# Kernel tuning notes

Measured on AMD Instinct MI355X. Metric: run time of the kernel, lower is better.

Reference implementation:

```python
import jax, jax.numpy as jnp
import numpy as np

N_NODES = 100000
N_EDGES = 3200000
NFEAT = 512
NHID = 256
KEEP_PROB = 0.5  # dropout p = 0.5


def setup_inputs() -> dict:
    key = jax.random.key(0)
    ks = jax.random.split(key, 9)
    x = jax.random.normal(ks[0], (N_NODES, NFEAT), dtype=jnp.float32)
    W1 = jax.random.normal(ks[1], (NFEAT, NHID), dtype=jnp.float32) * (1.0 / np.sqrt(NFEAT))
    b1 = jax.random.normal(ks[2], (NHID,), dtype=jnp.float32) * 0.01
    W2 = jax.random.normal(ks[3], (NHID, NHID), dtype=jnp.float32) * (1.0 / np.sqrt(NHID))
    b2 = jax.random.normal(ks[4], (NHID,), dtype=jnp.float32) * 0.01
    edge_row = jnp.sort(jax.random.randint(ks[5], (N_EDGES,), 0, N_NODES, dtype=jnp.int64))
    edge_col = jax.random.randint(ks[6], (N_EDGES,), 0, N_NODES, dtype=jnp.int64)
    edge_weight = jax.random.uniform(ks[7], (N_EDGES,), dtype=jnp.float32)
    drop_u = jax.random.uniform(ks[8], (N_NODES, NHID), dtype=jnp.float32)
    return {"x": x, "W1": W1, "b1": b1, "W2": W2, "b2": b2,
            "edge_row": edge_row, "edge_col": edge_col,
            "edge_weight": edge_weight, "drop_u": drop_u}


def reference(x, W1, b1, W2, b2, edge_row, edge_col, edge_weight, drop_u):
    n = x.shape[0]

    def spmm(h):
        # out[i] = sum_j adj[i, j] * h[j]  (COO gather + segment-sum)
        msg = h[edge_col] * edge_weight[:, None]  # [E, d]
        return jax.ops.segment_sum(msg, edge_row, num_segments=n)

    # layer 1: relu(spmm(adj, x @ W1) + b1)
    h = jax.nn.relu(spmm(x @ W1) + b1)
    # deterministic dropout (training=True, p=0.5): keep where u < keep_prob, scale by 1/keep
    mask = (drop_u < KEEP_PROB).astype(h.dtype)
    h = h * mask / KEEP_PROB
    # layer 2: relu(spmm(adj, h @ W2) + b2)
    h = jax.nn.relu(spmm(h @ W2) + b2)
    return jax.nn.log_softmax(h, axis=1)
```

## Files before the change

kernel.cpp:

```cpp
#include <hip/hip_runtime.h>
#include <stdint.h>

#define N_NODES 100000
#define N_EDGES 3200000
#define NFEAT 512
#define NHID 256
#define MPAD 100096

typedef __attribute__((ext_vector_type(8))) short bf16x8_t;
typedef __attribute__((ext_vector_type(4))) float f32x4_t;

#define RFL(x) __builtin_amdgcn_readfirstlane(x)

__device__ inline unsigned short f2bf(float f) {
  union { float f; uint32_t u; } x; x.f = f;
  uint32_t r = x.u + 0x7fffu + ((x.u >> 16) & 1u);
  return (unsigned short)(r >> 16);
}
__device__ inline float b2f(unsigned short u) {
  union { uint32_t u; float f; } x; x.u = ((uint32_t)u) << 16;
  return x.f;
}

__global__ void prep_k(const float* __restrict__ W1, const float* __restrict__ W2,
                       unsigned short* __restrict__ W1T, unsigned short* __restrict__ W2T) {
  int i = blockIdx.x * 256 + threadIdx.x;
  if (i < NFEAT * NHID) {
    int k = i >> 8, n = i & 255;
    W1T[n * NFEAT + k] = f2bf(W1[i]);
  } else {
    int j = i - NFEAT * NHID;
    int k = j >> 8, n = j & 255;
    W2T[n * NHID + k] = f2bf(W2[j]);
  }
}

__global__ void rowptr_k(const int* __restrict__ erow, int* __restrict__ rowptr) {
  int r = blockIdx.x * 256 + threadIdx.x;
  if (r > N_NODES) return;
  int lo = 0, hi = N_EDGES;
  while (lo < hi) {
    int mid = (lo + hi) >> 1;
    if (erow[mid] < r) lo = mid + 1; else hi = mid;
  }
  rowptr[r] = lo;
}

template <bool A_FP32>
__global__ __launch_bounds__(512) void gemm_bt2(const void* __restrict__ Ap,
                                                const unsigned short* __restrict__ BT,
                                                unsigned short* __restrict__ C,
                                                int K, int Mreal) {
  __shared__ __align__(16) unsigned short As[128 * 64];
  __shared__ __align__(16) unsigned short Bs[256 * 64];
  const int tid = threadIdx.x;
  const int lane = tid & 63, wid = tid >> 6;
  const int wm = wid >> 2, wn = wid & 3;
  const int m0 = blockIdx.x * 128;
  const int lrow = lane & 15, lhi = lane >> 4;

  f32x4_t acc[4][4] = {};

  const int nt = K >> 6;
  for (int t = 0; t < nt; ++t) {
    __syncthreads();
    if constexpr (A_FP32) {
      const float* A = (const float*)Ap;
      const int rr = tid >> 4;
      const int kq = (tid & 15) << 2;
#pragma unroll
      for (int round = 0; round < 4; ++round) {
        int row = rr + (round << 5);
        int grow = m0 + row; grow = grow < Mreal ? grow : Mreal - 1;
        const float4 v = *(const float4*)(A + (size_t)grow * K + (t << 6) + kq);
        ushort4 b4;
        b4.x = f2bf(v.x); b4.y = f2bf(v.y); b4.z = f2bf(v.z); b4.w = f2bf(v.w);
        *(ushort4*)&As[(row << 6) + (kq ^ ((row & 7) << 3))] = b4;
      }
    } else {
      const unsigned short* A = (const unsigned short*)Ap;
      const int Lrow = tid >> 3;
      const int Lc = (tid & 7) << 4;
#pragma unroll
      for (int round = 0; round < 2; ++round) {
        int row = Lrow + (round << 6);
        int srcc = Lc ^ ((row & 7) << 4);
        const char* g = (const char*)(A + (size_t)(m0 + row) * K + (t << 6)) + srcc;
        __builtin_amdgcn_global_load_lds(
            (const __attribute__((address_space(1))) void*)g,
            (__attribute__((address_space(3))) void*)((char*)As + tid * 16 + (round << 13)),
            16, 0, 0);
      }
    }
    {
      const int Lrow = tid >> 3;
      const int Lc = (tid & 7) << 4;
#pragma unroll
      for (int round = 0; round < 4; ++round) {
        int row = Lrow + (round << 6);
        int srcc = Lc ^ ((row & 7) << 4);
        const char* g = (const char*)(BT + (size_t)row * K + (t << 6)) + srcc;
        __builtin_amdgcn_global_load_lds(
            (const __attribute__((address_space(1))) void*)g,
            (__attribute__((address_space(3))) void*)((char*)Bs + tid * 16 + (round << 13)),
            16, 0, 0);
      }
    }
    asm volatile("s_waitcnt vmcnt(0)" ::: "memory");
    __syncthreads();

#pragma unroll
    for (int ks = 0; ks < 2; ++ks) {
      bf16x8_t af[4], bfr[4];
      const int cu = (ks << 5) + (lhi << 3);
#pragma unroll
      for (int mf = 0; mf < 4; ++mf) {
        int row = (wm << 6) + (mf << 4) + lrow;
        af[mf] = *(const bf16x8_t*)&As[(row << 6) + (cu ^ ((row & 7) << 3))];
      }
#pragma unroll
      for (int nf = 0; nf < 4; ++nf) {
        int row = (wn << 6) + (nf << 4) + lrow;
        bfr[nf] = *(const bf16x8_t*)&Bs[(row << 6) + (cu ^ ((row & 7) << 3))];
      }
#pragma unroll
      for (int mf = 0; mf < 4; ++mf)
#pragma unroll
        for (int nf = 0; nf < 4; ++nf)
          acc[mf][nf] = __builtin_amdgcn_mfma_f32_16x16x32_bf16(af[mf], bfr[nf], acc[mf][nf], 0, 0, 0);
    }
  }

#pragma unroll
  for (int mf = 0; mf < 4; ++mf)
#pragma unroll
    for (int nf = 0; nf < 4; ++nf)
#pragma unroll
      for (int j = 0; j < 4; ++j) {
        int gm = m0 + (wm << 6) + (mf << 4) + (lhi << 2) + j;
        int gn = (wn << 6) + (nf << 4) + lrow;
        C[(size_t)gm * 256 + gn] = f2bf(acc[mf][nf][j]);
      }
}

__global__ __launch_bounds__(256) void spmm1_k(const unsigned short* __restrict__ XW1,
                                               const int* __restrict__ rowptr,
                                               const int* __restrict__ ecol,
                                               const float* __restrict__ ew,
                                               const float* __restrict__ b1,
                                               const float* __restrict__ du,
                                               unsigned short* __restrict__ H) {
  const int lane = threadIdx.x & 63, wid = threadIdx.x >> 6;
  const int r = blockIdx.x * 4 + wid;
  const uint32_t c8 = (uint32_t)lane << 3;
  const int c4 = lane << 2;
  if (r >= N_NODES) {
    ushort4 z; z.x = z.y = z.z = z.w = 0;
    *(ushort4*)&H[(size_t)r * 256 + c4] = z;
    return;
  }
  const char* Xb = (const char*)XW1;
  const float4 bb = *(const float4*)&b1[c4];
  const float4 u = *(const float4*)&du[(size_t)r * 256 + c4];
  float a0 = 0, a1 = 0, a2 = 0, a3 = 0;
  int e  = RFL(rowptr[r]);
  int e1 = RFL(rowptr[r + 1]);
  for (; e + 8 <= e1; e += 8) {
    ushort4 v[8]; float w[8];
#pragma unroll
    for (int q = 0; q < 8; ++q) {
      uint32_t c = (uint32_t)RFL(ecol[e + q]);
      w[q] = __uint_as_float(RFL(__float_as_uint(ew[e + q])));
      v[q] = *(const ushort4*)(Xb + ((c << 9) + c8));
    }
#pragma unroll
    for (int q = 0; q < 8; ++q) {
      a0 += w[q] * b2f(v[q].x); a1 += w[q] * b2f(v[q].y);
      a2 += w[q] * b2f(v[q].z); a3 += w[q] * b2f(v[q].w);
    }
  }
  for (; e < e1; ++e) {
    uint32_t c = (uint32_t)RFL(ecol[e]);
    float w = __uint_as_float(RFL(__float_as_uint(ew[e])));
    ushort4 v = *(const ushort4*)(Xb + ((c << 9) + c8));
    a0 += w * b2f(v.x); a1 += w * b2f(v.y); a2 += w * b2f(v.z); a3 += w * b2f(v.w);
  }
  float h0 = fmaxf(a0 + bb.x, 0.f) * (u.x < 0.5f ? 2.f : 0.f);
  float h1 = fmaxf(a1 + bb.y, 0.f) * (u.y < 0.5f ? 2.f : 0.f);
  float h2 = fmaxf(a2 + bb.z, 0.f) * (u.z < 0.5f ? 2.f : 0.f);
  float h3 = fmaxf(a3 + bb.w, 0.f) * (u.w < 0.5f ? 2.f : 0.f);
  ushort4 o; o.x = f2bf(h0); o.y = f2bf(h1); o.z = f2bf(h2); o.w = f2bf(h3);
  *(ushort4*)&H[(size_t)r * 256 + c4] = o;
}

__global__ __launch_bounds__(256) void spmm2_k(const unsigned short* __restrict__ HW2,
                                               const int* __restrict__ rowptr,
                                               const int* __restrict__ ecol,
                                               const float* __restrict__ ew,
                                               const float* __restrict__ b2,
                                               float* __restrict__ out) {
  const int lane = threadIdx.x & 63, wid = threadIdx.x >> 6;
  const int r = blockIdx.x * 4 + wid;
  if (r >= N_NODES) return;
  const uint32_t c8 = (uint32_t)lane << 3;
  const int c4 = lane << 2;
  const char* Xb = (const char*)HW2;
  const float4 bb = *(const float4*)&b2[c4];
  float a0 = 0, a1 = 0, a2 = 0, a3 = 0;
  int e  = RFL(rowptr[r]);
  int e1 = RFL(rowptr[r + 1]);
  for (; e + 8 <= e1; e += 8) {
    ushort4 v[8]; float w[8];
#pragma unroll
    for (int q = 0; q < 8; ++q) {
      uint32_t c = (uint32_t)RFL(ecol[e + q]);
      w[q] = __uint_as_float(RFL(__float_as_uint(ew[e + q])));
      v[q] = *(const ushort4*)(Xb + ((c << 9) + c8));
    }
#pragma unroll
    for (int q = 0; q < 8; ++q) {
      a0 += w[q] * b2f(v[q].x); a1 += w[q] * b2f(v[q].y);
      a2 += w[q] * b2f(v[q].z); a3 += w[q] * b2f(v[q].w);
    }
  }
  for (; e < e1; ++e) {
    uint32_t c = (uint32_t)RFL(ecol[e]);
    float w = __uint_as_float(RFL(__float_as_uint(ew[e])));
    ushort4 v = *(const ushort4*)(Xb + ((c << 9) + c8));
    a0 += w * b2f(v.x); a1 += w * b2f(v.y); a2 += w * b2f(v.z); a3 += w * b2f(v.w);
  }
  float v0 = fmaxf(a0 + bb.x, 0.f);
  float v1 = fmaxf(a1 + bb.y, 0.f);
  float v2 = fmaxf(a2 + bb.z, 0.f);
  float v3 = fmaxf(a3 + bb.w, 0.f);
  float m = fmaxf(fmaxf(v0, v1), fmaxf(v2, v3));
#pragma unroll
  for (int off = 32; off > 0; off >>= 1) m = fmaxf(m, __shfl_xor(m, off));
  float s = expf(v0 - m) + expf(v1 - m) + expf(v2 - m) + expf(v3 - m);
#pragma unroll
  for (int off = 32; off > 0; off >>= 1) s += __shfl_xor(s, off);
  float ls = m + logf(s);
  float4 o; o.x = v0 - ls; o.y = v1 - ls; o.z = v2 - ls; o.w = v3 - ls;
  *(float4*)&out[(size_t)r * 256 + c4] = o;
}

extern "C" void kernel_launch(void* const* d_in, const int* in_sizes, int n_in,
                              void* d_out, int out_size, void* d_ws, size_t ws_size,
                              hipStream_t stream) {
  const float* x  = (const float*)d_in[0];
  const float* W1 = (const float*)d_in[1];
  const float* b1 = (const float*)d_in[2];
  const float* W2 = (const float*)d_in[3];
  const float* b2 = (const float*)d_in[4];
  const int* erow = (const int*)d_in[5];
  const int* ecol = (const int*)d_in[6];
  const float* ew = (const float*)d_in[7];
  const float* du = (const float*)d_in[8];
  float* out = (float*)d_out;

  char* ws = (char*)d_ws;
  unsigned short* W1T = (unsigned short*)ws;
  unsigned short* W2T = (unsigned short*)(ws + 262144);
  int* rowptr = (int*)(ws + 262144 + 131072);
  unsigned short* XW1 = (unsigned short*)(ws + 262144 + 131072 + 401408);
  unsigned short* H = (unsigned short*)(ws + 262144 + 131072 + 401408 + 51249152);

  prep_k<<<768, 256, 0, stream>>>(W1, W2, W1T, W2T);
  rowptr_k<<<392, 256, 0, stream>>>(erow, rowptr);
  gemm_bt2<true><<<782, 512, 0, stream>>>((const void*)x, W1T, XW1, NFEAT, N_NODES);
  spmm1_k<<<MPAD / 4, 256, 0, stream>>>(XW1, rowptr, ecol, ew, b1, du, H);
  gemm_bt2<false><<<782, 512, 0, stream>>>((const void*)H, W2T, XW1, NHID, MPAD);
  spmm2_k<<<N_NODES / 4, 256, 0, stream>>>(XW1, rowptr, ecol, ew, b2, out);
}
```

Measured before the change: 566.1 us.

## Double-buffer SpMM edge gathers and use nontemporal streaming loads and stores

The SpMM row loops now alternate two 8-edge register buffers, issuing the gathers for the next batch before accumulating the current one, so memory latency overlaps with the FMAs. Streaming data that is read or written once (x in the GEMM, dropout uniforms, final output) now goes through nontemporal loads and stores, which keeps the gathered feature rows resident in cache. The cost is roughly twice the registers for the gather buffers, which may lower occupancy.

```diff
diff --git a/kernel.cpp b/kernel.cpp
--- a/kernel.cpp
+++ b/kernel.cpp
@@ -72,7 +72,8 @@
       for (int round = 0; round < 4; ++round) {
         int row = rr + (round << 5);
         int grow = m0 + row; grow = grow < Mreal ? grow : Mreal - 1;
-        const float4 v = *(const float4*)(A + (size_t)grow * K + (t << 6) + kq);
+        const f32x4_t v = __builtin_nontemporal_load(
+            (const f32x4_t*)(A + (size_t)grow * K + (t << 6) + kq));
         ushort4 b4;
         b4.x = f2bf(v.x); b4.y = f2bf(v.y); b4.z = f2bf(v.z); b4.w = f2bf(v.w);
         *(ushort4*)&As[(row << 6) + (kq ^ ((row & 7) << 3))] = b4;
@@ -142,6 +143,20 @@
         C[(size_t)gm * 256 + gn] = f2bf(acc[mf][nf][j]);
       }
 }
+
+#define LOAD8(V, W, EB)                                              \
+  _Pragma("unroll")                                                  \
+  for (int q = 0; q < 8; ++q) {                                      \
+    uint32_t c = (uint32_t)RFL(ecol[(EB) + q]);                      \
+    W[q] = __uint_as_float(RFL(__float_as_uint(ew[(EB) + q])));      \
+    V[q] = *(const ushort4*)(Xb + ((c << 9) + c8));                  \
+  }
+#define CONS8(V, W)                                                  \
+  _Pragma("unroll")                                                  \
+  for (int q = 0; q < 8; ++q) {                                      \
+    a0 += W[q] * b2f(V[q].x); a1 += W[q] * b2f(V[q].y);              \
+    a2 += W[q] * b2f(V[q].z); a3 += W[q] * b2f(V[q].w);              \
+  }
 
 __global__ __launch_bounds__(256) void spmm1_k(const unsigned short* __restrict__ XW1,
                                                const int* __restrict__ rowptr,
@@ -161,22 +176,27 @@
   }
   const char* Xb = (const char*)XW1;
   const float4 bb = *(const float4*)&b1[c4];
-  const float4 u = *(const float4*)&du[(size_t)r * 256 + c4];
+  const f32x4_t u = __builtin_nontemporal_load((const f32x4_t*)&du[(size_t)r * 256 + c4]);
   float a0 = 0, a1 = 0, a2 = 0, a3 = 0;
   int e  = RFL(rowptr[r]);
-  int e1 = RFL(rowptr[r + 1]);
-  for (; e + 8 <= e1; e += 8) {
-    ushort4 v[8]; float w[8];
-#pragma unroll
-    for (int q = 0; q < 8; ++q) {
-      uint32_t c = (uint32_t)RFL(ecol[e + q]);
-      w[q] = __uint_as_float(RFL(__float_as_uint(ew[e + q])));
-      v[q] = *(const ushort4*)(Xb + ((c << 9) + c8));
-    }
-#pragma unroll
-    for (int q = 0; q < 8; ++q) {
-      a0 += w[q] * b2f(v[q].x); a1 += w[q] * b2f(v[q].y);
-      a2 += w[q] * b2f(v[q].z); a3 += w[q] * b2f(v[q].w);
+  const int e1 = RFL(rowptr[r + 1]);
+  ushort4 va[8], vb[8]; float wa[8], wb[8];
+  if (e + 8 <= e1) {
+    LOAD8(va, wa, e);
+    for (; e + 24 <= e1; e += 16) {
+      LOAD8(vb, wb, e + 8);
+      CONS8(va, wa);
+      LOAD8(va, wa, e + 16);
+      CONS8(vb, wb);
+    }
+    if (e + 16 <= e1) {
+      LOAD8(vb, wb, e + 8);
+      CONS8(va, wa);
+      CONS8(vb, wb);
+      e += 16;
+    } else {
+      CONS8(va, wa);
+      e += 8;
     }
   }
   for (; e < e1; ++e) {
@@ -208,19 +228,24 @@
   const float4 bb = *(const float4*)&b2[c4];
   float a0 = 0, a1 = 0, a2 = 0, a3 = 0;
   int e  = RFL(rowptr[r]);
-  int e1 = RFL(rowptr[r + 1]);
-  for (; e + 8 <= e1; e += 8) {
-    ushort4 v[8]; float w[8];
-#pragma unroll
-    for (int q = 0; q < 8; ++q) {
-      uint32_t c = (uint32_t)RFL(ecol[e + q]);
-      w[q] = __uint_as_float(RFL(__float_as_uint(ew[e + q])));
-      v[q] = *(const ushort4*)(Xb + ((c << 9) + c8));
-    }
-#pragma unroll
-    for (int q = 0; q < 8; ++q) {
-      a0 += w[q] * b2f(v[q].x); a1 += w[q] * b2f(v[q].y);
-      a2 += w[q] * b2f(v[q].z); a3 += w[q] * b2f(v[q].w);
+  const int e1 = RFL(rowptr[r + 1]);
+  ushort4 va[8], vb[8]; float wa[8], wb[8];
+  if (e + 8 <= e1) {
+    LOAD8(va, wa, e);
+    for (; e + 24 <= e1; e += 16) {
+      LOAD8(vb, wb, e + 8);
+      CONS8(va, wa);
+      LOAD8(va, wa, e + 16);
+      CONS8(vb, wb);
+    }
+    if (e + 16 <= e1) {
+      LOAD8(vb, wb, e + 8);
+      CONS8(va, wa);
+      CONS8(vb, wb);
+      e += 16;
+    } else {
+      CONS8(va, wa);
+      e += 8;
     }
   }
   for (; e < e1; ++e) {
@@ -240,8 +265,8 @@
 #pragma unroll
   for (int off = 32; off > 0; off >>= 1) s += __shfl_xor(s, off);
   float ls = m + logf(s);
-  float4 o; o.x = v0 - ls; o.y = v1 - ls; o.z = v2 - ls; o.w = v3 - ls;
-  *(float4*)&out[(size_t)r * 256 + c4] = o;
+  f32x4_t o; o.x = v0 - ls; o.y = v1 - ls; o.z = v2 - ls; o.w = v3 - ls;
+  __builtin_nontemporal_store(o, (f32x4_t*)&out[(size_t)r * 256 + c4]);
 }
 
 extern "C" void kernel_launch(void* const* d_in, const int* in_sizes, int n_in,
```

After: 550.1 us. 1.03x faster.

## Split wave into two half-waves gathering alternate edges with 16-byte loads

Applied to the files above, without the earlier changes.

Both SpMM kernels now have each half of the wavefront handle alternate edges. Each lane loads 8 bf16 values (16 bytes) instead of 4, and the two halves are combined with a cross-lane shuffle at the end. The gather loop is software-pipelined with double-buffered register sets, so the next group of edge loads is issued before the current group is consumed. Nontemporal loads and stores are also used for streaming data (x in the GEMM, the dropout uniforms, the final output). The gather should issue fewer, wider memory requests per row, at the cost of higher register pressure and a reduction step.

```diff
diff --git a/kernel.cpp b/kernel.cpp
--- a/kernel.cpp
+++ b/kernel.cpp
@@ -8,6 +8,7 @@
 #define MPAD 100096
 
 typedef __attribute__((ext_vector_type(8))) short bf16x8_t;
+typedef __attribute__((ext_vector_type(8))) unsigned short u16x8_t;
 typedef __attribute__((ext_vector_type(4))) float f32x4_t;
 
 #define RFL(x) __builtin_amdgcn_readfirstlane(x)
@@ -72,7 +73,8 @@
       for (int round = 0; round < 4; ++round) {
         int row = rr + (round << 5);
         int grow = m0 + row; grow = grow < Mreal ? grow : Mreal - 1;
-        const float4 v = *(const float4*)(A + (size_t)grow * K + (t << 6) + kq);
+        const f32x4_t v = __builtin_nontemporal_load(
+            (const f32x4_t*)(A + (size_t)grow * K + (t << 6) + kq));
         ushort4 b4;
         b4.x = f2bf(v.x); b4.y = f2bf(v.y); b4.z = f2bf(v.z); b4.w = f2bf(v.w);
         *(ushort4*)&As[(row << 6) + (kq ^ ((row & 7) << 3))] = b4;
@@ -142,6 +144,52 @@
         C[(size_t)gm * 256 + gn] = f2bf(acc[mf][nf][j]);
       }
 }
+
+#define LOADP4(V, W, EB)                                             \
+  _Pragma("unroll")                                                  \
+  for (int q = 0; q < 4; ++q) {                                      \
+    uint32_t ce = (uint32_t)RFL(ecol[(EB) + 2 * q]);                 \
+    uint32_t co = (uint32_t)RFL(ecol[(EB) + 2 * q + 1]);             \
+    uint32_t ue = RFL(__float_as_uint(ew[(EB) + 2 * q]));            \
+    uint32_t uo = RFL(__float_as_uint(ew[(EB) + 2 * q + 1]));        \
+    uint32_t cv = lo ? ce : co;                                      \
+    W[q] = __uint_as_float(lo ? ue : uo);                            \
+    V[q] = *(const u16x8_t*)(Xb + (((size_t)cv << 9) + c16));        \
+  }
+#define CONSP4(V, W)                                                 \
+  _Pragma("unroll")                                                  \
+  for (int q = 0; q < 4; ++q)                                        \
+    _Pragma("unroll")                                                \
+    for (int j = 0; j < 8; ++j)                                      \
+      f[j] += W[q] * b2f(V[q][j]);
+
+#define GATHER_ROW()                                                 \
+  u16x8_t va[4], vb[4]; float wa[4], wb[4];                          \
+  if (e + 8 <= e1) {                                                 \
+    LOADP4(va, wa, e);                                               \
+    for (; e + 24 <= e1; e += 16) {                                  \
+      LOADP4(vb, wb, e + 8);                                         \
+      CONSP4(va, wa);                                                \
+      LOADP4(va, wa, e + 16);                                        \
+      CONSP4(vb, wb);                                                \
+    }                                                                \
+    if (e + 16 <= e1) {                                              \
+      LOADP4(vb, wb, e + 8);                                         \
+      CONSP4(va, wa);                                                \
+      CONSP4(vb, wb);                                                \
+      e += 16;                                                       \
+    } else { CONSP4(va, wa); e += 8; }                               \
+  }                                                                  \
+  for (; e < e1; ++e) {         \
+    uint32_t c = (uint32_t)RFL(ecol[e]);                             \
+    float w = __uint_as_float(RFL(__float_as_uint(ew[e])));          \
+    u16x8_t v = *(const u16x8_t*)(Xb + (((size_t)c << 9) + c16));    \
+    float wv = lo ? w : 0.0f;                                        \
+    _Pragma("unroll")                                                \
+    for (int j = 0; j < 8; ++j) f[j] += wv * b2f(v[j]);              \
+  }                                                                  \
+  _Pragma("unroll")                                                  \
+  for (int j = 0; j < 8; ++j) f[j] += __shfl_xor(f[j], 32);
 
 __global__ __launch_bounds__(256) void spmm1_k(const unsigned short* __restrict__ XW1,
                                                const int* __restrict__ rowptr,
@@ -152,45 +200,38 @@
                                                unsigned short* __restrict__ H) {
   const int lane = threadIdx.x & 63, wid = threadIdx.x >> 6;
   const int r = blockIdx.x * 4 + wid;
-  const uint32_t c8 = (uint32_t)lane << 3;
-  const int c4 = lane << 2;
+  const bool lo = lane < 32;
+  const int g = lane & 31;
+  const uint32_t c16 = (uint32_t)g << 4;
   if (r >= N_NODES) {
-    ushort4 z; z.x = z.y = z.z = z.w = 0;
-    *(ushort4*)&H[(size_t)r * 256 + c4] = z;
+    if (lo) {
+      u16x8_t z;
+#pragma unroll
+      for (int j = 0; j < 8; ++j) z[j] = 0;
+      *(u16x8_t*)&H[(size_t)r * 256 + (g << 3)] = z;
+    }
     return;
   }
   const char* Xb = (const char*)XW1;
-  const float4 bb = *(const float4*)&b1[c4];
-  const float4 u = *(const float4*)&du[(size_t)r * 256 + c4];
-  float a0 = 0, a1 = 0, a2 = 0, a3 = 0;
+  float f[8] = {};
   int e  = RFL(rowptr[r]);
-  int e1 = RFL(rowptr[r + 1]);
-  for (; e + 8 <= e1; e += 8) {
-    ushort4 v[8]; float w[8];
-#pragma unroll
-    for (int q = 0; q < 8; ++q) {
-      uint32_t c = (uint32_t)RFL(ecol[e + q]);
-      w[q] = __uint_as_float(RFL(__float_as_uint(ew[e + q])));
-      v[q] = *(const ushort4*)(Xb + ((c << 9) + c8));
-    }
-#pragma unroll
-    for (int q = 0; q < 8; ++q) {
-      a0 += w[q] * b2f(v[q].x); a1 += w[q] * b2f(v[q].y);
-      a2 += w[q] * b2f(v[q].z); a3 += w[q] * b2f(v[q].w);
-    }
-  }
-  for (; e < e1; ++e) {
-    uint32_t c = (uint32_t)RFL(ecol[e]);
-    float w = __uint_as_float(RFL(__float_as_uint(ew[e])));
-    ushort4 v = *(const ushort4*)(Xb + ((c << 9) + c8));
-    a0 += w * b2f(v.x); a1 += w * b2f(v.y); a2 += w * b2f(v.z); a3 += w * b2f(v.w);
-  }
-  float h0 = fmaxf(a0 + bb.x, 0.f) * (u.x < 0.5f ? 2.f : 0.f);
-  float h1 = fmaxf(a1 + bb.y, 0.f) * (u.y < 0.5f ? 2.f : 0.f);
-  float h2 = fmaxf(a2 + bb.z, 0.f) * (u.z < 0.5f ? 2.f : 0.f);
-  float h3 = fmaxf(a3 + bb.w, 0.f) * (u.w < 0.5f ? 2.f : 0.f);
-  ushort4 o; o.x = f2bf(h0); o.y = f2bf(h1); o.z = f2bf(h2); o.w = f2bf(h3);
-  *(ushort4*)&H[(size_t)r * 256 + c4] = o;
+  const int e1 = RFL(rowptr[r + 1]);
+  GATHER_ROW();
+  if (lo) {
+    const int g8 = g << 3;
+    float bv[8], uu[8];
+    *(f32x4_t*)&bv[0] = *(const f32x4_t*)&b1[g8];
+    *(f32x4_t*)&bv[4] = *(const f32x4_t*)&b1[g8 + 4];
+    *(f32x4_t*)&uu[0] = __builtin_nontemporal_load((const f32x4_t*)&du[(size_t)r * 256 + g8]);
+    *(f32x4_t*)&uu[4] = __builtin_nontemporal_load((const f32x4_t*)&du[(size_t)r * 256 + g8 + 4]);
+    u16x8_t o;
+#pragma unroll
+    for (int j = 0; j < 8; ++j) {
+      float h = fmaxf(f[j] + bv[j], 0.f) * (uu[j] < 0.5f ? 2.f : 0.f);
+      o[j] = f2bf(h);
+    }
+    *(u16x8_t*)&H[(size_t)r * 256 + g8] = o;
+  }
 }
 
 __global__ __launch_bounds__(256) void spmm2_k(const unsigned short* __restrict__ HW2,
@@ -202,46 +243,39 @@
   const int lane = threadIdx.x & 63, wid = threadIdx.x >> 6;
   const int r = blockIdx.x * 4 + wid;
   if (r >= N_NODES) return;
-  const uint32_t c8 = (uint32_t)lane << 3;
-  const int c4 = lane << 2;
+  const bool lo = lane < 32;
+  const int g = lane & 31;
+  const uint32_t c16 = (uint32_t)g << 4;
   const char* Xb = (const char*)HW2;
-  const float4 bb = *(const float4*)&b2[c4];
-  float a0 = 0, a1 = 0, a2 = 0, a3 = 0;
+  float f[8] = {};
   int e  = RFL(rowptr[r]);
-  int e1 = RFL(rowptr[r + 1]);
-  for (; e + 8 <= e1; e += 8) {
-    ushort4 v[8]; float w[8];
-#pragma unroll
-    for (int q = 0; q < 8; ++q) {
-      uint32_t c = (uint32_t)RFL(ecol[e + q]);
-      w[q] = __uint_as_float(RFL(__float_as_uint(ew[e + q])));
-      v[q] = *(const ushort4*)(Xb + ((c << 9) + c8));
-    }
-#pragma unroll
-    for (int q = 0; q < 8; ++q) {
-      a0 += w[q] * b2f(v[q].x); a1 += w[q] * b2f(v[q].y);
-      a2 += w[q] * b2f(v[q].z); a3 += w[q] * b2f(v[q].w);
-    }
-  }
-  for (; e < e1; ++e) {
-    uint32_t c = (uint32_t)RFL(ecol[e]);
-    float w = __uint_as_float(RFL(__float_as_uint(ew[e])));
-    ushort4 v = *(const ushort4*)(Xb + ((c << 9) + c8));
-    a0 += w * b2f(v.x); a1 += w * b2f(v.y); a2 += w * b2f(v.z); a3 += w * b2f(v.w);
-  }
-  float v0 = fmaxf(a0 + bb.x, 0.f);
-  float v1 = fmaxf(a1 + bb.y, 0.f);
-  float v2 = fmaxf(a2 + bb.z, 0.f);
-  float v3 = fmaxf(a3 + bb.w, 0.f);
-  float m = fmaxf(fmaxf(v0, v1), fmaxf(v2, v3));
-#pragma unroll
-  for (int off = 32; off > 0; off >>= 1) m = fmaxf(m, __shfl_xor(m, off));
-  float s = expf(v0 - m) + expf(v1 - m) + expf(v2 - m) + expf(v3 - m);
-#pragma unroll
-  for (int off = 32; off > 0; off >>= 1) s += __shfl_xor(s, off);
-  float ls = m + logf(s);
-  float4 o; o.x = v0 - ls; o.y = v1 - ls; o.z = v2 - ls; o.w = v3 - ls;
-  *(float4*)&out[(size_t)r * 256 + c4] = o;
+  const int e1 = RFL(rowptr[r + 1]);
+  GATHER_ROW();
+  const int g8 = g << 3;
+  float bv[8];
+  *(f32x4_t*)&bv[0] = *(const f32x4_t*)&b2[g8];
+  *(f32x4_t*)&bv[4] = *(const f32x4_t*)&b2[g8 + 4];
+  float v[8];
+#pragma unroll
+  for (int j = 0; j < 8; ++j) v[j] = fmaxf(f[j] + bv[j], 0.f);
+  float m = v[0];
+#pragma unroll
+  for (int j = 1; j < 8; ++j) m = fmaxf(m, v[j]);
+#pragma unroll
+  for (int off = 16; off > 0; off >>= 1) m = fmaxf(m, __shfl_xor(m, off));
+  float s = 0.f;
+#pragma unroll
+  for (int j = 0; j < 8; ++j) s += expf(v[j] - m);
+#pragma unroll
+  for (int off = 16; off > 0; off >>= 1) s += __shfl_xor(s, off);
+  const float ls = m + logf(s);
+  if (lo) {
+    f32x4_t o0, o1;
+    o0.x = v[0] - ls; o0.y = v[1] - ls; o0.z = v[2] - ls; o0.w = v[3] - ls;
+    o1.x = v[4] - ls; o1.y = v[5] - ls; o1.z = v[6] - ls; o1.w = v[7] - ls;
+    __builtin_nontemporal_store(o0, (f32x4_t*)&out[(size_t)r * 256 + g8]);
+    __builtin_nontemporal_store(o1, (f32x4_t*)&out[(size_t)r * 256 + g8 + 4]);
+  }
 }
 
 extern "C" void kernel_launch(void* const* d_in, const int* in_sizes, int n_in,
```

After: 547.6 us. 1.03x faster.
